# Performance work log

Measured on AMD Instinct MI355X. Metric: run time of the kernel, lower is better.

## Reference

```python
import jax, jax.numpy as jnp
import numpy as np

K = 4096          # infeatures
N = 11008         # outfeatures
GROUPSIZE = 128
NG = K // GROUPSIZE  # number of quantization groups
B, S = 2, 2048


def setup_inputs() -> dict:
    key = jax.random.key(0)
    k1, k2, k3, k4, k5 = jax.random.split(key, 5)
    x = jax.random.normal(k1, (B, S, K), dtype=jnp.float32)

    shifts = jnp.arange(8, dtype=jnp.int32) * 4
    # pack 8 int4 nibbles per int32 along the K (row) axis, GPTQ-style
    nib = jax.random.randint(k2, (K, N), 0, 16, dtype=jnp.int32)
    qweight = jnp.sum(nib.reshape(K // 8, 8, N) << shifts[None, :, None], axis=1).astype(jnp.int32)
    # pack 8 int4 zero-points per int32 along the N (col) axis
    znib = jax.random.randint(k3, (NG, N), 0, 16, dtype=jnp.int32)
    qzeros = jnp.sum(znib.reshape(NG, N // 8, 8) << shifts[None, None, :], axis=2).astype(jnp.int32)

    scales = jax.random.uniform(k4, (NG, N), dtype=jnp.float32, minval=1e-3, maxval=1e-2)
    g_idx = (jnp.arange(K) // GROUPSIZE).astype(jnp.int32)
    bias = jax.random.normal(k5, (N,), dtype=jnp.float32) * 0.01
    return {"x": x, "qweight": qweight, "qzeros": qzeros, "scales": scales,
            "g_idx": g_idx, "bias": bias}


def _dequantize(qweight, qzeros, scales, g_idx):
    shifts = jnp.arange(8, dtype=jnp.int32) * 4
    # unpack int4 weights: row r of W comes from qweight[r // 8], nibble r % 8
    q = ((qweight[:, None, :] >> shifts[None, :, None]) & 0xF).reshape(K, N)
    # unpack int4 zero-points (GPTQ stores zero-1, so add 1 back)
    z = (((qzeros[:, :, None] >> shifts[None, None, :]) & 0xF) + 1).reshape(NG, N)
    return (q - z[g_idx]).astype(scales.dtype) * scales[g_idx]  # [K, N]


def reference(x, qweight, qzeros, scales, g_idx, bias):
    W = _dequantize(qweight, qzeros, scales, g_idx)
    return jnp.einsum('bsk,kn->bsn', x, W) + bias
```

## Files before the change

kernel.cpp:

```cpp
#include <hip/hip_runtime.h>

#define M_DIM 4096
#define K_DIM 4096
#define N_DIM 11008
#define GS 128

typedef _Float16 half8 __attribute__((ext_vector_type(8)));
typedef _Float16 half4 __attribute__((ext_vector_type(4)));
typedef _Float16 half2v __attribute__((ext_vector_type(2)));
typedef float f32x4 __attribute__((ext_vector_type(4)));

#define AH_BYTES 33554432ull
#define WT_BYTES 90177536ull

__global__ __launch_bounds__(256) void cvtA_kernel(const float4* __restrict__ x4,
                                                   half8* __restrict__ a8) {
    int i = blockIdx.x * 256 + threadIdx.x;
    float4 u = x4[2 * i];
    float4 v = x4[2 * i + 1];
    half8 h;
    h[0] = (_Float16)u.x; h[1] = (_Float16)u.y; h[2] = (_Float16)u.z; h[3] = (_Float16)u.w;
    h[4] = (_Float16)v.x; h[5] = (_Float16)v.y; h[6] = (_Float16)v.z; h[7] = (_Float16)v.w;
    a8[i] = h;
}

__global__ __launch_bounds__(256) void dequantW2_kernel(const int* __restrict__ qw,
                                                        const int* __restrict__ qz,
                                                        const float* __restrict__ sc,
                                                        _Float16* __restrict__ Wt) {
    const int b   = blockIdx.x;
    const int nb  = (b % 344) * 32;
    const int kwb = (b / 344) * 8;
    const int t   = threadIdx.x;
    const int l   = t & 63;
    const int n   = nb + (t >> 6) * 8 + (l >> 3);
    const int kw  = kwb + (l & 7);
    const int g   = kwb >> 4;

    float s = sc[(size_t)g * N_DIM + n];
    int zw = qz[(size_t)g * (N_DIM / 8) + (n >> 3)];
    int z  = ((zw >> ((n & 7) * 4)) & 0xF) + 1;
    _Float16 sh  = (_Float16)s;
    _Float16 zsh = (_Float16)(-(float)z * s);
    half2v s2 = {sh, sh}, zs2 = {zsh, zsh};
    const half2v c1024 = {(_Float16)1024.0f, (_Float16)1024.0f};

    unsigned q = (unsigned)qw[(size_t)kw * N_DIM + n];
    half2v p[4];
    #pragma unroll
    for (int jj = 0; jj < 4; ++jj) {
        unsigned tt = ((q >> (4 * jj)) & 0x000F000Fu) | 0x64006400u;
        half2v h = __builtin_bit_cast(half2v, tt);
        h = h - c1024;
        p[jj] = h * s2 + zs2;
    }
    half8 wv;
    wv[0] = p[0][0]; wv[1] = p[1][0]; wv[2] = p[2][0]; wv[3] = p[3][0];
    wv[4] = p[0][1]; wv[5] = p[1][1]; wv[6] = p[2][1]; wv[7] = p[3][1];
    *(half8*)(Wt + (size_t)n * K_DIM + (size_t)kw * 8) = wv;
}


#define SWZ(r) ((((r) >> 1) & 3) << 4)

#define VMC3() asm volatile("s_waitcnt vmcnt(3)" ::: "memory")
#define VMC0() asm volatile("s_waitcnt vmcnt(0)" ::: "memory")
#define VMCN()

#define STAGE3(TT, SB) do {                                                           \
    char* db_ = smem + (SB) * 24576;                                                  \
    __builtin_amdgcn_global_load_lds(                                                 \
        (const __attribute__((address_space(1))) void*)(ahb + srcA0 + (size_t)(TT) * 64), \
        (__attribute__((address_space(3))) void*)(db_ + wid * 1024), 16, 0, 0);       \
    __builtin_amdgcn_global_load_lds(                                                 \
        (const __attribute__((address_space(1))) void*)(ahb + srcA1 + (size_t)(TT) * 64), \
        (__attribute__((address_space(3))) void*)(db_ + 8192 + wid * 1024), 16, 0, 0);\
    __builtin_amdgcn_global_load_lds(                                                 \
        (const __attribute__((address_space(1))) void*)(wtb + srcB0 + (size_t)(TT) * 64), \
        (__attribute__((address_space(3))) void*)(db_ + 16384 + wid * 1024), 16, 0, 0);\
} while (0)

#define BODY(CB, SB, STT, STG, VMC) do {                                              \
    const char* Ab_ = smem + (CB) * 24576;                                            \
    half8 af0 = *(const half8*)(Ab_ + aoff_0);                                        \
    half8 af1 = *(const half8*)(Ab_ + aoff_1);                                        \
    half8 af2 = *(const half8*)(Ab_ + aoff_2);                                        \
    half8 af3 = *(const half8*)(Ab_ + aoff_3);                                        \
    half8 bf0 = *(const half8*)(Ab_ + boff_0);                                        \
    half8 bf1 = *(const half8*)(Ab_ + boff_1);                                        \
    half8 bf2 = *(const half8*)(Ab_ + boff_2);                                        \
    half8 bf3 = *(const half8*)(Ab_ + boff_3);                                        \
    if (STG) { STAGE3((STT), (SB)); }                                                 \
    VMC();                                                                            \
    __builtin_amdgcn_s_barrier();                                                     \
    asm volatile("s_waitcnt lgkmcnt(0)" ::: "memory");                                \
    __builtin_amdgcn_sched_barrier(0);                                                \
    __builtin_amdgcn_s_setprio(1);                                                    \
    acc[0][0] = __builtin_amdgcn_mfma_f32_16x16x32_f16(af0, bf0, acc[0][0], 0, 0, 0); \
    acc[0][1] = __builtin_amdgcn_mfma_f32_16x16x32_f16(af0, bf1, acc[0][1], 0, 0, 0); \
    acc[0][2] = __builtin_amdgcn_mfma_f32_16x16x32_f16(af0, bf2, acc[0][2], 0, 0, 0); \
    acc[0][3] = __builtin_amdgcn_mfma_f32_16x16x32_f16(af0, bf3, acc[0][3], 0, 0, 0); \
    acc[1][0] = __builtin_amdgcn_mfma_f32_16x16x32_f16(af1, bf0, acc[1][0], 0, 0, 0); \
    acc[1][1] = __builtin_amdgcn_mfma_f32_16x16x32_f16(af1, bf1, acc[1][1], 0, 0, 0); \
    acc[1][2] = __builtin_amdgcn_mfma_f32_16x16x32_f16(af1, bf2, acc[1][2], 0, 0, 0); \
    acc[1][3] = __builtin_amdgcn_mfma_f32_16x16x32_f16(af1, bf3, acc[1][3], 0, 0, 0); \
    acc[2][0] = __builtin_amdgcn_mfma_f32_16x16x32_f16(af2, bf0, acc[2][0], 0, 0, 0); \
    acc[2][1] = __builtin_amdgcn_mfma_f32_16x16x32_f16(af2, bf1, acc[2][1], 0, 0, 0); \
    acc[2][2] = __builtin_amdgcn_mfma_f32_16x16x32_f16(af2, bf2, acc[2][2], 0, 0, 0); \
    acc[2][3] = __builtin_amdgcn_mfma_f32_16x16x32_f16(af2, bf3, acc[2][3], 0, 0, 0); \
    acc[3][0] = __builtin_amdgcn_mfma_f32_16x16x32_f16(af3, bf0, acc[3][0], 0, 0, 0); \
    acc[3][1] = __builtin_amdgcn_mfma_f32_16x16x32_f16(af3, bf1, acc[3][1], 0, 0, 0); \
    acc[3][2] = __builtin_amdgcn_mfma_f32_16x16x32_f16(af3, bf2, acc[3][2], 0, 0, 0); \
    acc[3][3] = __builtin_amdgcn_mfma_f32_16x16x32_f16(af3, bf3, acc[3][3], 0, 0, 0); \
    __builtin_amdgcn_s_setprio(0);                                                    \
    __builtin_amdgcn_s_barrier();                                                     \
} while (0)

__global__ __launch_bounds__(512, 4) void gemm9_kernel(
    const _Float16* __restrict__ Ah,
    const _Float16* __restrict__ Wt,
    const float* __restrict__ bias,
    float* __restrict__ out)
{
    extern __shared__ char smem[];

    const int tid  = threadIdx.x;
    const int lane = tid & 63;
    const int wid  = tid >> 6;
    const int wr   = wid >> 1;
    const int wc   = wid & 1;

    int orig = blockIdx.x;
    int wg = (orig & 7) * 172 + (orig >> 3);
    const int tm = wg / 86;
    const int tn = wg - tm * 86;
    const int m0 = tm * 256;
    const int n0 = tn * 128;

    const char* ahb = (const char*)Ah;
    const char* wtb = (const char*)Wt;

    const int rS  = wid * 16 + (lane >> 2);
    const int kbS = ((lane & 3) << 4) ^ SWZ(rS);
    const size_t srcA0 = ((size_t)(m0 + rS) << 13) + kbS;
    const size_t srcA1 = ((size_t)(m0 + rS + 128) << 13) + kbS;
    const size_t srcB0 = ((size_t)(n0 + rS) << 13) + kbS;

    const int klane = (lane >> 4) << 4;
    int ra, aoff_0, aoff_1, aoff_2, aoff_3, boff_0, boff_1, boff_2, boff_3;
    ra = wr * 64 +  0 + (lane & 15); aoff_0 = ra * 64 + (klane ^ SWZ(ra));
    ra = wr * 64 + 16 + (lane & 15); aoff_1 = ra * 64 + (klane ^ SWZ(ra));
    ra = wr * 64 + 32 + (lane & 15); aoff_2 = ra * 64 + (klane ^ SWZ(ra));
    ra = wr * 64 + 48 + (lane & 15); aoff_3 = ra * 64 + (klane ^ SWZ(ra));
    ra = wc * 64 +  0 + (lane & 15); boff_0 = 16384 + ra * 64 + (klane ^ SWZ(ra));
    ra = wc * 64 + 16 + (lane & 15); boff_1 = 16384 + ra * 64 + (klane ^ SWZ(ra));
    ra = wc * 64 + 32 + (lane & 15); boff_2 = 16384 + ra * 64 + (klane ^ SWZ(ra));
    ra = wc * 64 + 48 + (lane & 15); boff_3 = 16384 + ra * 64 + (klane ^ SWZ(ra));

    f32x4 acc[4][4];
    #pragma unroll
    for (int i = 0; i < 4; ++i)
        #pragma unroll
        for (int j = 0; j < 4; ++j)
            acc[i][j] = f32x4{0.f, 0.f, 0.f, 0.f};

    STAGE3(0, 0);
    STAGE3(1, 1);
    VMC3();
    __builtin_amdgcn_s_barrier();

    for (int it = 0; it < 42; ++it) {
        const int T = 3 * it;
        BODY(0, 2, T + 2, 1, VMC3);
        BODY(1, 0, T + 3, 1, VMC3);
        BODY(2, 1, T + 4, 1, VMC3);
    }
    BODY(0, 2, 0, 0, VMC0);
    BODY(1, 0, 0, 0, VMCN);

    const int row_base = m0 + wr * 64 + ((lane >> 4) << 2);
    const int col_base = n0 + wc * 64 + (lane & 15);
    #pragma unroll
    for (int ni = 0; ni < 4; ++ni) {
        const int col = col_base + ni * 16;
        const float bv = bias[col];
        #pragma unroll
        for (int mi = 0; mi < 4; ++mi) {
            const int row = row_base + mi * 16;
            #pragma unroll
            for (int j = 0; j < 4; ++j)
                out[(size_t)(row + j) * N_DIM + col] = acc[mi][ni][j] + bv;
        }
    }
}

__global__ __launch_bounds__(256, 2) void gptq_fallback_kernel(
    const float* __restrict__ x, const int* __restrict__ qw, const int* __restrict__ qz,
    const float* __restrict__ sc, const float* __restrict__ bias, float* __restrict__ out)
{
    __shared__ _Float16 As[128 * 64];
    __shared__ _Float16 Bs[128 * 64];
    const int tid = threadIdx.x, lane = tid & 63, wid = tid >> 6;
    const int wr = wid >> 1, wc = wid & 1;
    int orig = blockIdx.x;
    int wg = (orig & 7) * 344 + (orig >> 3);
    const int tm = wg / 86, tn = wg - tm * 86;
    const int m0 = tm * 128, n0 = tn * 128;
    const int a_r0 = tid >> 4, a_c4 = tid & 15;
    const int b_nl = tid & 127, b_qr0 = tid >> 7, b_n = n0 + b_nl;
    const float* xg = x + (size_t)(m0 + a_r0) * K_DIM + a_c4 * 4;
    const int* qwg = qw + (size_t)b_qr0 * N_DIM + b_n;
    float4 areg[8]; int breg[4]; float s_cur, zs_cur;
    #pragma unroll
    for (int i = 0; i < 8; ++i) areg[i] = *(const float4*)(xg + (size_t)i * 16 * K_DIM);
    #pragma unroll
    for (int i = 0; i < 4; ++i) breg[i] = qwg[(size_t)i * 2 * N_DIM];
    { int zw = qz[(size_t)(b_n >> 3)]; int z = ((zw >> ((b_n & 7) * 4)) & 0xF) + 1;
      float s = sc[b_n]; s_cur = s; zs_cur = -(float)z * s; }
    f32x4 acc[4][4];
    #pragma unroll
    for (int i = 0; i < 4; ++i)
        #pragma unroll
        for (int j = 0; j < 4; ++j) acc[i][j] = f32x4{0.f,0.f,0.f,0.f};
    const half2v c1024 = {(_Float16)1024.0f, (_Float16)1024.0f};
    for (int kt = 0; kt < 64; ++kt) {
        if (kt) __syncthreads();
        #pragma unroll
        for (int i = 0; i < 8; ++i) {
            int r = i * 16 + a_r0;
            half4 hv; hv[0]=(_Float16)areg[i].x; hv[1]=(_Float16)areg[i].y;
            hv[2]=(_Float16)areg[i].z; hv[3]=(_Float16)areg[i].w;
            int boff = ((r * 64 + a_c4 * 4) * 2) ^ ((r & 7) << 4);
            *(half4*)((char*)As + boff) = hv;
        }
        { _Float16 sh=(_Float16)s_cur, zsh=(_Float16)zs_cur;
          half2v s2={sh,sh}, zs2={zsh,zsh};
          #pragma unroll
          for (int i = 0; i < 4; ++i) {
            unsigned q = (unsigned)breg[i]; half2v p[4];
            #pragma unroll
            for (int j = 0; j < 4; ++j) {
                unsigned t = ((q >> (4*j)) & 0x000F000Fu) | 0x64006400u;
                half2v h = __builtin_bit_cast(half2v, t); h = h - c1024;
                p[j] = h * s2 + zs2;
            }
            half8 wv; wv[0]=p[0][0]; wv[1]=p[1][0]; wv[2]=p[2][0]; wv[3]=p[3][0];
            wv[4]=p[0][1]; wv[5]=p[1][1]; wv[6]=p[2][1]; wv[7]=p[3][1];
            int qr = b_qr0 + i * 2;
            int boff = ((b_nl * 64 + qr * 8) * 2) ^ ((b_nl & 7) << 4);
            *(half8*)((char*)Bs + boff) = wv;
          } }
        __syncthreads();
        if (kt + 1 < 64) {
            const float* xg2 = xg + (size_t)(kt + 1) * 64;
            #pragma unroll
            for (int i = 0; i < 8; ++i) areg[i] = *(const float4*)(xg2 + (size_t)i * 16 * K_DIM);
            const int* qwg2 = qwg + (size_t)(kt + 1) * 8 * N_DIM;
            #pragma unroll
            for (int i = 0; i < 4; ++i) breg[i] = qwg2[(size_t)i * 2 * N_DIM];
            int g = ((kt + 1) * 64) / GS;
            int zw = qz[(size_t)g * (N_DIM / 8) + (b_n >> 3)];
            int z = ((zw >> ((b_n & 7) * 4)) & 0xF) + 1;
            float s = sc[(size_t)g * N_DIM + b_n];
            s_cur = s; zs_cur = -(float)z * s;
        }
        #pragma unroll
        for (int ks = 0; ks < 2; ++ks) {
            half8 af[4], bf[4];
            int kb = ks * 64 + ((lane >> 4) * 16);
            #pragma unroll
            for (int mi = 0; mi < 4; ++mi) {
                int r = wr * 64 + mi * 16 + (lane & 15);
                int boff = (r * 128 + kb) ^ ((r & 7) << 4);
                af[mi] = *(const half8*)((const char*)As + boff);
            }
            #pragma unroll
            for (int ni = 0; ni < 4; ++ni) {
                int c = wc * 64 + ni * 16 + (lane & 15);
                int boff = (c * 128 + kb) ^ ((c & 7) << 4);
                bf[ni] = *(const half8*)((const char*)Bs + boff);
            }
            #pragma unroll
            for (int mi = 0; mi < 4; ++mi)
                #pragma unroll
                for (int ni = 0; ni < 4; ++ni)
                    acc[mi][ni] = __builtin_amdgcn_mfma_f32_16x16x32_f16(af[mi], bf[ni], acc[mi][ni], 0, 0, 0);
        }
    }
    const int col_base = n0 + wc * 64 + (lane & 15);
    const int row_base = m0 + wr * 64 + ((lane >> 4) << 2);
    #pragma unroll
    for (int ni = 0; ni < 4; ++ni) {
        int col = col_base + ni * 16;
        float bv = bias[col];
        #pragma unroll
        for (int mi = 0; mi < 4; ++mi) {
            int row = row_base + mi * 16;
            #pragma unroll
            for (int j = 0; j < 4; ++j)
                out[(size_t)(row + j) * N_DIM + col] = acc[mi][ni][j] + bv;
        }
    }
}

extern "C" void kernel_launch(void* const* d_in, const int* in_sizes, int n_in,
                              void* d_out, int out_size, void* d_ws, size_t ws_size,
                              hipStream_t stream) {
    const float* x    = (const float*)d_in[0];
    const int*   qw   = (const int*)d_in[1];
    const int*   qz   = (const int*)d_in[2];
    const float* sc   = (const float*)d_in[3];
    const float* bias = (const float*)d_in[5];
    float* out = (float*)d_out;

    if (ws_size >= AH_BYTES + WT_BYTES) {
        _Float16* Ah = (_Float16*)d_ws;
        _Float16* Wt = (_Float16*)((char*)d_ws + AH_BYTES);
        cvtA_kernel<<<8192, 256, 0, stream>>>((const float4*)x, (half8*)Ah);
        dequantW2_kernel<<<344 * 64, 256, 0, stream>>>(qw, qz, sc, Wt);
        (void)hipFuncSetAttribute((const void*)gemm9_kernel,
                                  hipFuncAttributeMaxDynamicSharedMemorySize, 73728);
        gemm9_kernel<<<1376, 512, 73728, stream>>>(Ah, Wt, bias, out);
    } else {
        gptq_fallback_kernel<<<2752, 256, 0, stream>>>(x, qw, qz, sc, bias, out);
    }
}
```

Baseline: 633.4 us.

## Enlarge GEMM tile to 256x256 with K=64 double-buffered half-tile staging

Replaces the 256x128, K=32 triple-buffered GEMM with a 256x256 output tile per workgroup, K-step 64, and two 64KB LDS buffers. Each K tile is split into four quarter-phases with interleaved global->LDS staging of the next tile's halves, using an XOR swizzle. The larger tile halves redundant A traffic and raises MFMA work per LDS byte. In exchange it uses 128 accumulator registers per lane and 128KB of LDS, lowers occupancy, and launches 688 blocks instead of 1376, which may reduce wave-level parallelism. It also adds more barriers per tile.

```diff
diff --git a/kernel.cpp b/kernel.cpp
--- a/kernel.cpp
+++ b/kernel.cpp
@@ -4,14 +4,17 @@
 #define K_DIM 4096
 #define N_DIM 11008
 #define GS 128
+#define NKT 64
 
 typedef _Float16 half8 __attribute__((ext_vector_type(8)));
-typedef _Float16 half4 __attribute__((ext_vector_type(4)));
 typedef _Float16 half2v __attribute__((ext_vector_type(2)));
 typedef float f32x4 __attribute__((ext_vector_type(4)));
 
 #define AH_BYTES 33554432ull
 #define WT_BYTES 90177536ull
+
+#define AS1 __attribute__((address_space(1)))
+#define AS3 __attribute__((address_space(3)))
 
 __global__ __launch_bounds__(256) void cvtA_kernel(const float4* __restrict__ x4,
                                                    half8* __restrict__ a8) {
@@ -61,62 +64,68 @@
 }
 
 
-#define SWZ(r) ((((r) >> 1) & 3) << 4)
-
-#define VMC3() asm volatile("s_waitcnt vmcnt(3)" ::: "memory")
-#define VMC0() asm volatile("s_waitcnt vmcnt(0)" ::: "memory")
+#define BAR()   __builtin_amdgcn_s_barrier()
+#define LGKM0() do { asm volatile("s_waitcnt lgkmcnt(0)" ::: "memory"); \
+                     __builtin_amdgcn_sched_barrier(0); } while (0)
+#define VMC4()  asm volatile("s_waitcnt vmcnt(4)" ::: "memory")
+#define VMC0()  asm volatile("s_waitcnt vmcnt(0)" ::: "memory")
 #define VMCN()
 
-#define STAGE3(TT, SB) do {                                                           \
-    char* db_ = smem + (SB) * 24576;                                                  \
-    __builtin_amdgcn_global_load_lds(                                                 \
-        (const __attribute__((address_space(1))) void*)(ahb + srcA0 + (size_t)(TT) * 64), \
-        (__attribute__((address_space(3))) void*)(db_ + wid * 1024), 16, 0, 0);       \
-    __builtin_amdgcn_global_load_lds(                                                 \
-        (const __attribute__((address_space(1))) void*)(ahb + srcA1 + (size_t)(TT) * 64), \
-        (__attribute__((address_space(3))) void*)(db_ + 8192 + wid * 1024), 16, 0, 0);\
-    __builtin_amdgcn_global_load_lds(                                                 \
-        (const __attribute__((address_space(1))) void*)(wtb + srcB0 + (size_t)(TT) * 64), \
-        (__attribute__((address_space(3))) void*)(db_ + 16384 + wid * 1024), 16, 0, 0);\
+#define LDA(cb, MH) \
+    _Pragma("unroll") \
+    for (int mi = 0; mi < 4; ++mi) { \
+        aF[mi][0] = *(const half8*)(smem + (cb)*65536 + arow + (MH)*8192 + mi*2048 + koff0); \
+        aF[mi][1] = *(const half8*)(smem + (cb)*65536 + arow + (MH)*8192 + mi*2048 + koff1); \
+    }
+
+#define LDB(cb, NH, BF) \
+    _Pragma("unroll") \
+    for (int ni = 0; ni < 2; ++ni) { \
+        BF[ni][0] = *(const half8*)(smem + (cb)*65536 + brow + (NH)*4096 + ni*2048 + koff0); \
+        BF[ni][1] = *(const half8*)(smem + (cb)*65536 + brow + (NH)*4096 + ni*2048 + koff1); \
+    }
+
+#define MM(MB, NB, BF) \
+    _Pragma("unroll") \
+    for (int kh = 0; kh < 2; ++kh) \
+    _Pragma("unroll") \
+    for (int mi = 0; mi < 4; ++mi) \
+    _Pragma("unroll") \
+    for (int ni = 0; ni < 2; ++ni) \
+        acc[(MB)+mi][(NB)+ni] = __builtin_amdgcn_mfma_f32_16x16x32_f16( \
+            aF[mi][kh], BF[ni][kh], acc[(MB)+mi][(NB)+ni], 0, 0, 0)
+
+#define STAGE_HT(OB, HT, BASE, T) do { \
+    __builtin_amdgcn_global_load_lds((const AS1 void*)((BASE) + (size_t)(T)*128), \
+        (AS3 void*)(smem + (OB)*65536 + (HT)*16384 + tid*16), 16, 0, 0); \
+    __builtin_amdgcn_global_load_lds((const AS1 void*)((BASE) + (size_t)(T)*128 + 524288), \
+        (AS3 void*)(smem + (OB)*65536 + (HT)*16384 + 8192 + tid*16), 16, 0, 0); \
 } while (0)
 
-#define BODY(CB, SB, STT, STG, VMC) do {                                              \
-    const char* Ab_ = smem + (CB) * 24576;                                            \
-    half8 af0 = *(const half8*)(Ab_ + aoff_0);                                        \
-    half8 af1 = *(const half8*)(Ab_ + aoff_1);                                        \
-    half8 af2 = *(const half8*)(Ab_ + aoff_2);                                        \
-    half8 af3 = *(const half8*)(Ab_ + aoff_3);                                        \
-    half8 bf0 = *(const half8*)(Ab_ + boff_0);                                        \
-    half8 bf1 = *(const half8*)(Ab_ + boff_1);                                        \
-    half8 bf2 = *(const half8*)(Ab_ + boff_2);                                        \
-    half8 bf3 = *(const half8*)(Ab_ + boff_3);                                        \
-    if (STG) { STAGE3((STT), (SB)); }                                                 \
-    VMC();                                                                            \
-    __builtin_amdgcn_s_barrier();                                                     \
-    asm volatile("s_waitcnt lgkmcnt(0)" ::: "memory");                                \
-    __builtin_amdgcn_sched_barrier(0);                                                \
-    __builtin_amdgcn_s_setprio(1);                                                    \
-    acc[0][0] = __builtin_amdgcn_mfma_f32_16x16x32_f16(af0, bf0, acc[0][0], 0, 0, 0); \
-    acc[0][1] = __builtin_amdgcn_mfma_f32_16x16x32_f16(af0, bf1, acc[0][1], 0, 0, 0); \
-    acc[0][2] = __builtin_amdgcn_mfma_f32_16x16x32_f16(af0, bf2, acc[0][2], 0, 0, 0); \
-    acc[0][3] = __builtin_amdgcn_mfma_f32_16x16x32_f16(af0, bf3, acc[0][3], 0, 0, 0); \
-    acc[1][0] = __builtin_amdgcn_mfma_f32_16x16x32_f16(af1, bf0, acc[1][0], 0, 0, 0); \
-    acc[1][1] = __builtin_amdgcn_mfma_f32_16x16x32_f16(af1, bf1, acc[1][1], 0, 0, 0); \
-    acc[1][2] = __builtin_amdgcn_mfma_f32_16x16x32_f16(af1, bf2, acc[1][2], 0, 0, 0); \
-    acc[1][3] = __builtin_amdgcn_mfma_f32_16x16x32_f16(af1, bf3, acc[1][3], 0, 0, 0); \
-    acc[2][0] = __builtin_amdgcn_mfma_f32_16x16x32_f16(af2, bf0, acc[2][0], 0, 0, 0); \
-    acc[2][1] = __builtin_amdgcn_mfma_f32_16x16x32_f16(af2, bf1, acc[2][1], 0, 0, 0); \
-    acc[2][2] = __builtin_amdgcn_mfma_f32_16x16x32_f16(af2, bf2, acc[2][2], 0, 0, 0); \
-    acc[2][3] = __builtin_amdgcn_mfma_f32_16x16x32_f16(af2, bf3, acc[2][3], 0, 0, 0); \
-    acc[3][0] = __builtin_amdgcn_mfma_f32_16x16x32_f16(af3, bf0, acc[3][0], 0, 0, 0); \
-    acc[3][1] = __builtin_amdgcn_mfma_f32_16x16x32_f16(af3, bf1, acc[3][1], 0, 0, 0); \
-    acc[3][2] = __builtin_amdgcn_mfma_f32_16x16x32_f16(af3, bf2, acc[3][2], 0, 0, 0); \
-    acc[3][3] = __builtin_amdgcn_mfma_f32_16x16x32_f16(af3, bf3, acc[3][3], 0, 0, 0); \
-    __builtin_amdgcn_s_setprio(0);                                                    \
-    __builtin_amdgcn_s_barrier();                                                     \
+#define TILE(cb, T, S01, S23, VMC) do {                                   \
+    LDA(cb, 0); LDB(cb, 0, bF0);                                          \
+    if (S01) STAGE_HT((cb)^1, 1, pA1, (T)+1);                             \
+    BAR(); LGKM0();                                                       \
+    __builtin_amdgcn_s_setprio(1); MM(0, 0, bF0);                         \
+    __builtin_amdgcn_s_setprio(0); BAR();                                 \
+    LDB(cb, 1, bF1);                                                      \
+    if (S01) STAGE_HT((cb)^1, 3, pB1, (T)+1);                             \
+    BAR(); LGKM0();                                                       \
+    __builtin_amdgcn_s_setprio(1); MM(0, 2, bF1);                         \
+    __builtin_amdgcn_s_setprio(0); BAR();                                 \
+    LDA(cb, 1);                                                           \
+    if (S23) STAGE_HT((cb), 2, pB0, (T)+2);                               \
+    BAR(); LGKM0();                                                       \
+    __builtin_amdgcn_s_setprio(1); MM(4, 2, bF1);                         \
+    __builtin_amdgcn_s_setprio(0); BAR();                                 \
+    if (S23) STAGE_HT((cb), 0, pA0, (T)+2);                               \
+    VMC();                                                                \
+    BAR();                                                                \
+    __builtin_amdgcn_s_setprio(1); MM(4, 0, bF0);                         \
+    __builtin_amdgcn_s_setprio(0); BAR();                                 \
 } while (0)
 
-__global__ __launch_bounds__(512, 4) void gemm9_kernel(
+__global__ __launch_bounds__(512, 2) void gemm10_kernel(
     const _Float16* __restrict__ Ah,
     const _Float16* __restrict__ Wt,
     const float* __restrict__ bias,
@@ -127,65 +136,60 @@
     const int tid  = threadIdx.x;
     const int lane = tid & 63;
     const int wid  = tid >> 6;
-    const int wr   = wid >> 1;
-    const int wc   = wid & 1;
+    const int wr   = wid >> 2;
+    const int wc   = wid & 3;
 
     int orig = blockIdx.x;
-    int wg = (orig & 7) * 172 + (orig >> 3);
-    const int tm = wg / 86;
-    const int tn = wg - tm * 86;
+    int wg = (orig & 7) * 86 + (orig >> 3);
+    const int tm = wg / 43;
+    const int tn = wg - tm * 43;
     const int m0 = tm * 256;
-    const int n0 = tn * 128;
-
-    const char* ahb = (const char*)Ah;
-    const char* wtb = (const char*)Wt;
-
-    const int rS  = wid * 16 + (lane >> 2);
-    const int kbS = ((lane & 3) << 4) ^ SWZ(rS);
-    const size_t srcA0 = ((size_t)(m0 + rS) << 13) + kbS;
-    const size_t srcA1 = ((size_t)(m0 + rS + 128) << 13) + kbS;
-    const size_t srcB0 = ((size_t)(n0 + rS) << 13) + kbS;
-
-    const int klane = (lane >> 4) << 4;
-    int ra, aoff_0, aoff_1, aoff_2, aoff_3, boff_0, boff_1, boff_2, boff_3;
-    ra = wr * 64 +  0 + (lane & 15); aoff_0 = ra * 64 + (klane ^ SWZ(ra));
-    ra = wr * 64 + 16 + (lane & 15); aoff_1 = ra * 64 + (klane ^ SWZ(ra));
-    ra = wr * 64 + 32 + (lane & 15); aoff_2 = ra * 64 + (klane ^ SWZ(ra));
-    ra = wr * 64 + 48 + (lane & 15); aoff_3 = ra * 64 + (klane ^ SWZ(ra));
-    ra = wc * 64 +  0 + (lane & 15); boff_0 = 16384 + ra * 64 + (klane ^ SWZ(ra));
-    ra = wc * 64 + 16 + (lane & 15); boff_1 = 16384 + ra * 64 + (klane ^ SWZ(ra));
-    ra = wc * 64 + 32 + (lane & 15); boff_2 = 16384 + ra * 64 + (klane ^ SWZ(ra));
-    ra = wc * 64 + 48 + (lane & 15); boff_3 = 16384 + ra * 64 + (klane ^ SWZ(ra));
-
-    f32x4 acc[4][4];
-    #pragma unroll
-    for (int i = 0; i < 4; ++i)
+    const int n0 = tn * 256;
+
+    const int koff0 = 16 * (((lane >> 4) + 0) ^ (lane & 7));
+    const int koff1 = 16 * (((lane >> 4) + 4) ^ (lane & 7));
+    const int arow  = (wr * 128 + (lane & 15)) * 128;
+    const int brow  = 32768 + (wc * 64 + (lane & 15)) * 128;
+
+    const int sb = ((tid & 7) * 16) ^ (((tid >> 3) & 7) << 4);
+    const char* pA0 = (const char*)Ah + (size_t)(m0 + (tid >> 3)) * 8192 + sb;
+    const char* pA1 = pA0 + 1048576;
+    const char* pB0 = (const char*)Wt + (size_t)(n0 + (tid >> 3)) * 8192 + sb;
+    const char* pB1 = pB0 + 1048576;
+
+    half8 aF[4][2], bF0[2][2], bF1[2][2];
+    f32x4 acc[8][4];
+    #pragma unroll
+    for (int i = 0; i < 8; ++i)
         #pragma unroll
         for (int j = 0; j < 4; ++j)
             acc[i][j] = f32x4{0.f, 0.f, 0.f, 0.f};
 
-    STAGE3(0, 0);
-    STAGE3(1, 1);
-    VMC3();
-    __builtin_amdgcn_s_barrier();
-
-    for (int it = 0; it < 42; ++it) {
-        const int T = 3 * it;
-        BODY(0, 2, T + 2, 1, VMC3);
-        BODY(1, 0, T + 3, 1, VMC3);
-        BODY(2, 1, T + 4, 1, VMC3);
-    }
-    BODY(0, 2, 0, 0, VMC0);
-    BODY(1, 0, 0, 0, VMCN);
-
-    const int row_base = m0 + wr * 64 + ((lane >> 4) << 2);
+    STAGE_HT(0, 0, pA0, 0);
+    STAGE_HT(0, 1, pA1, 0);
+    STAGE_HT(0, 2, pB0, 0);
+    STAGE_HT(0, 3, pB1, 0);
+    STAGE_HT(1, 2, pB0, 1);
+    STAGE_HT(1, 0, pA0, 1);
+    VMC4();
+    BAR();
+
+    for (int t2 = 0; t2 < 31; ++t2) {
+        const int T = 2 * t2;
+        TILE(0, T,     1, 1, VMC4);
+        TILE(1, T + 1, 1, 1, VMC4);
+    }
+    TILE(0, 62, 1, 0, VMC0);
+    TILE(1, 63, 0, 0, VMCN);
+
+    const int row_base = m0 + wr * 128 + ((lane >> 4) << 2);
     const int col_base = n0 + wc * 64 + (lane & 15);
     #pragma unroll
     for (int ni = 0; ni < 4; ++ni) {
         const int col = col_base + ni * 16;
         const float bv = bias[col];
         #pragma unroll
-        for (int mi = 0; mi < 4; ++mi) {
+        for (int mi = 0; mi < 8; ++mi) {
             const int row = row_base + mi * 16;
             #pragma unroll
             for (int j = 0; j < 4; ++j)
@@ -228,10 +232,12 @@
         #pragma unroll
         for (int i = 0; i < 8; ++i) {
             int r = i * 16 + a_r0;
-            half4 hv; hv[0]=(_Float16)areg[i].x; hv[1]=(_Float16)areg[i].y;
-            hv[2]=(_Float16)areg[i].z; hv[3]=(_Float16)areg[i].w;
+            half2v hv0, hv1;
+            hv0[0]=(_Float16)areg[i].x; hv0[1]=(_Float16)areg[i].y;
+            hv1[0]=(_Float16)areg[i].z; hv1[1]=(_Float16)areg[i].w;
             int boff = ((r * 64 + a_c4 * 4) * 2) ^ ((r & 7) << 4);
-            *(half4*)((char*)As + boff) = hv;
+            *(half2v*)((char*)As + boff) = hv0;
+            *(half2v*)((char*)As + boff + 4) = hv1;
         }
         { _Float16 sh=(_Float16)s_cur, zsh=(_Float16)zs_cur;
           half2v s2={sh,sh}, zs2={zsh,zsh};
@@ -318,9 +324,9 @@
         _Float16* Wt = (_Float16*)((char*)d_ws + AH_BYTES);
         cvtA_kernel<<<8192, 256, 0, stream>>>((const float4*)x, (half8*)Ah);
         dequantW2_kernel<<<344 * 64, 256, 0, stream>>>(qw, qz, sc, Wt);
-        (void)hipFuncSetAttribute((const void*)gemm9_kernel,
-                                  hipFuncAttributeMaxDynamicSharedMemorySize, 73728);
-        gemm9_kernel<<<1376, 512, 73728, stream>>>(Ah, Wt, bias, out);
+        (void)hipFuncSetAttribute((const void*)gemm10_kernel,
+                                  hipFuncAttributeMaxDynamicSharedMemorySize, 131072);
+        gemm10_kernel<<<688, 512, 131072, stream>>>(Ah, Wt, bias, out);
     } else {
         gptq_fallback_kernel<<<2752, 256, 0, stream>>>(x, qw, qz, sc, bias, out);
     }
```

Result: faster. 597.2 us (-5.7%).
